# Performance work log

Hardware: AMD Instinct MI355X
Metric: run time of the kernel (lower is better)

Reference implementation:

```python
import jax, jax.numpy as jnp
import numpy as np

PLANE_SIZE = 512
N_LEVELS = 8
FEATURE_DIM = 16
N_PTS = 524288


def setup_inputs() -> dict:
    key = jax.random.key(0)
    k1, k2, k3 = jax.random.split(key, 3)
    x = jax.random.uniform(k1, (N_PTS, 3), dtype=jnp.float32)
    # per-point float mip level bias in [0, n_levels-1]
    level = jax.random.uniform(k2, (N_PTS, 1), dtype=jnp.float32) * (N_LEVELS - 1)
    fm = jax.random.uniform(k3, (3, PLANE_SIZE, PLANE_SIZE, FEATURE_DIM),
                            minval=-0.01, maxval=0.01, dtype=jnp.float32)
    return {"x": x, "level": level, "fm": fm, "n_levels": N_LEVELS}


def _bilinear(flat_pyr, offsets, sizes, uv, lvl_i):
    # flat_pyr: (3, T, C) concatenated mip levels; uv: (3, N, 2); lvl_i: (3, N) int32
    size = sizes[lvl_i]                      # (3, N) texture size at this mip
    fsize = size.astype(uv.dtype)
    px = uv[..., 0] * fsize - 0.5            # u -> width axis (nvdiffrast convention)
    py = uv[..., 1] * fsize - 0.5            # v -> height axis
    x0 = jnp.floor(px)
    y0 = jnp.floor(py)
    fx = (px - x0)[..., None]
    fy = (py - y0)[..., None]
    x0i = x0.astype(jnp.int32)
    y0i = y0.astype(jnp.int32)
    xa = jnp.clip(x0i, 0, size - 1)          # boundary_mode='clamp'
    xb = jnp.clip(x0i + 1, 0, size - 1)
    ya = jnp.clip(y0i, 0, size - 1)
    yb = jnp.clip(y0i + 1, 0, size - 1)
    base = offsets[lvl_i]
    p = jnp.arange(3)[:, None]
    g = lambda yy, xx: flat_pyr[p, base + yy * size + xx]   # (3, N, C) gather
    f00 = g(ya, xa); f01 = g(ya, xb); f10 = g(yb, xa); f11 = g(yb, xb)
    return (f00 * (1 - fx) + f01 * fx) * (1 - fy) + (f10 * (1 - fx) + f11 * fx) * fy


def reference(x, level, fm, n_levels):
    N = x.shape[0]
    C = fm.shape[-1]
    # build mip pyramid via 2x2 box filter (nvdiffrast auto-mips)
    levels = [fm]
    for _ in range(n_levels - 1):
        t = levels[-1]
        s = t.shape[1]
        levels.append(t.reshape(3, s // 2, 2, s // 2, 2, C).mean(axis=(2, 4)))
    sizes_list = [l.shape[1] for l in levels]
    offsets = jnp.asarray(np.cumsum([0] + [s * s for s in sizes_list[:-1]]), jnp.int32)
    sizes = jnp.asarray(sizes_list, jnp.int32)
    flat_pyr = jnp.concatenate([l.reshape(3, -1, C) for l in levels], axis=1)  # (3, T, C)
    # tri-plane decomposition: plane0 sees (y,z), plane1 (x,z), plane2 (x,y)
    uv = jnp.stack([x[:, [1, 2]], x[:, [0, 2]], x[:, [0, 1]]], axis=0)  # (3, N, 2)
    max_mip = n_levels - 1
    lvl = jnp.clip(jnp.broadcast_to(level.reshape(1, N), (3, N)), 0.0, float(max_mip))
    l0 = jnp.floor(lvl)
    f = (lvl - l0)[..., None]                # (3, N, 1) level fraction
    l0i = l0.astype(jnp.int32)
    l1i = jnp.minimum(l0i + 1, max_mip)
    s0 = _bilinear(flat_pyr, offsets, sizes, uv, l0i)
    s1 = _bilinear(flat_pyr, offsets, sizes, uv, l1i)
    enc = s0 * (1 - f) + s1 * f              # (3, N, C) trilinear (mip-lerped)
    # permute(1,2,0,3).view(N, 3C): per point, concat plane0|plane1|plane2 features
    return jnp.transpose(enc, (1, 0, 2)).reshape(N, 3 * C)
```

## Files before the change

kernel.cpp:

```cpp
#include <hip/hip_runtime.h>


#define FM_PLANE_STRIDE (262144 * 16)
#define WS_PLANE_STRIDE (87376 * 16)

__device__ __forceinline__ float4 ld4(const float* p) {
    return *reinterpret_cast<const float4*>(p);
}
__device__ __forceinline__ void st4(float* p, float4 v) {
    *reinterpret_cast<float4*>(p) = v;
}
__device__ __forceinline__ float4 avg4(float4 a, float4 b, float4 c, float4 d) {
    float4 r;
    r.x = (a.x + b.x + c.x + d.x) * 0.25f;
    r.y = (a.y + b.y + c.y + d.y) * 0.25f;
    r.z = (a.z + b.z + c.z + d.z) * 0.25f;
    r.w = (a.w + b.w + c.w + d.w) * 0.25f;
    return r;
}

__global__ __launch_bounds__(256) void mip_build(
    const float* __restrict__ src, float* __restrict__ dst)
{
    const int s = 256;
    int t = blockIdx.x * blockDim.x + threadIdx.x;
    const int p = blockIdx.y;
    const int q = t & 3;
    const int idx = t >> 2;
    const int y = idx >> 8;
    const int x = idx & 255;
    const int ss = 512;
    const float* sp = src + (size_t)p * FM_PLANE_STRIDE
                          + ((size_t)(2 * y) * ss + 2 * x) * 16 + q * 4;
    float4 a = ld4(sp);
    float4 b = ld4(sp + 16);
    float4 c = ld4(sp + (size_t)ss * 16);
    float4 d = ld4(sp + (size_t)ss * 16 + 16);
    float* dp = dst + (size_t)p * WS_PLANE_STRIDE + ((size_t)y * s + x) * 16 + q * 4;
    st4(dp, avg4(a, b, c, d));
}

__global__ __launch_bounds__(256) void mip_tail(float* __restrict__ mips)
{
    const int tile = blockIdx.x;
    const int q    = blockIdx.y;
    const int p    = blockIdx.z;
    const int ty = tile >> 2, tx = tile & 3;
    const int tid = threadIdx.x;

    __shared__ float4 A[32 * 32];
    __shared__ float4 B[16 * 16];

    float* plane = mips + (size_t)p * WS_PLANE_STRIDE;
    const float* L1 = plane;
    float* L2 = plane + (size_t)65536 * 16;
    float* L3 = plane + (size_t)81920 * 16;
    float* L4 = plane + (size_t)86016 * 16;
    float* L5 = plane + (size_t)87040 * 16;
    float* L6 = plane + (size_t)87296 * 16;
    float* L7 = plane + (size_t)87360 * 16;

    #pragma unroll
    for (int k = 0; k < 4; ++k) {
        int li = tid + k * 256;
        int ly = li >> 5, lx = li & 31;
        int gy = ty * 32 + ly, gx = tx * 32 + lx;
        const float* sp = L1 + ((size_t)(2 * gy) * 256 + 2 * gx) * 16 + q * 4;
        float4 r = avg4(ld4(sp), ld4(sp + 16),
                        ld4(sp + 256 * 16), ld4(sp + 256 * 16 + 16));
        A[li] = r;
        st4(L2 + ((size_t)gy * 128 + gx) * 16 + q * 4, r);
    }
    __syncthreads();

    if (tid < 256) {
        int ly = tid >> 4, lx = tid & 15;
        float4 r = avg4(A[(2 * ly) * 32 + 2 * lx],     A[(2 * ly) * 32 + 2 * lx + 1],
                        A[(2 * ly + 1) * 32 + 2 * lx], A[(2 * ly + 1) * 32 + 2 * lx + 1]);
        B[tid] = r;
        st4(L3 + ((size_t)(ty * 16 + ly) * 64 + tx * 16 + lx) * 16 + q * 4, r);
    }
    __syncthreads();

    if (tid < 64) {
        int ly = tid >> 3, lx = tid & 7;
        float4 r = avg4(B[(2 * ly) * 16 + 2 * lx],     B[(2 * ly) * 16 + 2 * lx + 1],
                        B[(2 * ly + 1) * 16 + 2 * lx], B[(2 * ly + 1) * 16 + 2 * lx + 1]);
        A[tid] = r;
        st4(L4 + ((size_t)(ty * 8 + ly) * 32 + tx * 8 + lx) * 16 + q * 4, r);
    }
    __syncthreads();

    if (tid < 16) {
        int ly = tid >> 2, lx = tid & 3;
        float4 r = avg4(A[(2 * ly) * 8 + 2 * lx],     A[(2 * ly) * 8 + 2 * lx + 1],
                        A[(2 * ly + 1) * 8 + 2 * lx], A[(2 * ly + 1) * 8 + 2 * lx + 1]);
        B[tid] = r;
        st4(L5 + ((size_t)(ty * 4 + ly) * 16 + tx * 4 + lx) * 16 + q * 4, r);
    }
    __syncthreads();

    if (tid < 4) {
        int ly = tid >> 1, lx = tid & 1;
        float4 r = avg4(B[(2 * ly) * 4 + 2 * lx],     B[(2 * ly) * 4 + 2 * lx + 1],
                        B[(2 * ly + 1) * 4 + 2 * lx], B[(2 * ly + 1) * 4 + 2 * lx + 1]);
        A[tid] = r;
        st4(L6 + ((size_t)(ty * 2 + ly) * 8 + tx * 2 + lx) * 16 + q * 4, r);
    }
    __syncthreads();

    if (tid == 0) {
        float4 r = avg4(A[0], A[1], A[2], A[3]);
        st4(L7 + ((size_t)ty * 4 + tx) * 16 + q * 4, r);
    }
}

__device__ __forceinline__ float4 bilerp(
    const float* __restrict__ fm, const float* __restrict__ mips,
    int p, int l, float u, float v, int q)
{
    const int sz = 512 >> l;
    const float fsz = (float)sz;
    float px = u * fsz - 0.5f;
    float py = v * fsz - 0.5f;
    float xf = floorf(px);
    float yf = floorf(py);
    float fx = px - xf;
    float fy = py - yf;
    int xi = (int)xf;
    int yi = (int)yf;
    int xa = min(max(xi, 0), sz - 1);
    int xb = min(xi + 1, sz - 1);
    int ya = min(max(yi, 0), sz - 1);
    int yb = min(yi + 1, sz - 1);
    const float* base;
    if (l == 0) {
        base = fm + (size_t)p * FM_PLANE_STRIDE;
    } else {
        unsigned off = (262144u - ((unsigned)(sz * sz) << 2)) / 3u;
        base = mips + (size_t)p * WS_PLANE_STRIDE + (size_t)off * 16;
    }
    const float* r0 = base + (size_t)(ya * sz) * 16 + q * 4;
    const float* r1 = base + (size_t)(yb * sz) * 16 + q * 4;
    float4 f00 = ld4(r0 + xa * 16);
    float4 f01 = ld4(r0 + xb * 16);
    float4 f10 = ld4(r1 + xa * 16);
    float4 f11 = ld4(r1 + xb * 16);
    float gx = 1.f - fx, gy = 1.f - fy;
    float4 r;
    r.x = (f00.x * gx + f01.x * fx) * gy + (f10.x * gx + f11.x * fx) * fy;
    r.y = (f00.y * gx + f01.y * fx) * gy + (f10.y * gx + f11.y * fx) * fy;
    r.z = (f00.z * gx + f01.z * fx) * gy + (f10.z * gx + f11.z * fx) * fy;
    r.w = (f00.w * gx + f01.w * fx) * gy + (f10.w * gx + f11.w * fx) * fy;
    return r;
}

__global__ __launch_bounds__(256) void trimip_sample(
    const float* __restrict__ xyz, const float* __restrict__ level,
    const float* __restrict__ fm, const float* __restrict__ mips,
    float* __restrict__ out, int N)
{
    int t = blockIdx.x * blockDim.x + threadIdx.x;
    if (t >= N * 12) return;
    const int q = t & 3;
    const int r = t >> 2;
    const int n = r / 3;
    const int p = r - n * 3;

    const float c0 = xyz[n * 3 + 0];
    const float c1 = xyz[n * 3 + 1];
    const float c2 = xyz[n * 3 + 2];
    const float u = (p == 0) ? c1 : c0;
    const float v = (p == 2) ? c1 : c2;

    float lv = level[n];
    lv = fminf(fmaxf(lv, 0.f), 7.f);
    float lf = floorf(lv);
    float f = lv - lf;
    int l0 = (int)lf;
    int l1 = min(l0 + 1, 7);

    float4 s0 = bilerp(fm, mips, p, l0, u, v, q);
    float4 s1 = bilerp(fm, mips, p, l1, u, v, q);
    float g = 1.f - f;
    float4 o;
    o.x = s0.x * g + s1.x * f;
    o.y = s0.y * g + s1.y * f;
    o.z = s0.z * g + s1.z * f;
    o.w = s0.w * g + s1.w * f;
    reinterpret_cast<float4*>(out)[t] = o;
}

extern "C" void kernel_launch(void* const* d_in, const int* in_sizes, int n_in,
                              void* d_out, int out_size, void* d_ws, size_t ws_size,
                              hipStream_t stream) {
    const float* xyz   = (const float*)d_in[0];
    const float* level = (const float*)d_in[1];
    const float* fm    = (const float*)d_in[2];
    float* mips = (float*)d_ws;
    float* out  = (float*)d_out;
    const int N = in_sizes[1];

    mip_build<<<dim3(1024, 3), dim3(256), 0, stream>>>(fm, mips);
    mip_tail<<<dim3(16, 4, 3), dim3(256), 0, stream>>>(mips);

    const int total = N * 12;
    const int blocks = (total + 255) / 256;
    trimip_sample<<<blocks, 256, 0, stream>>>(xyz, level, fm, mips, out, N);
}
```

Baseline: 211.2 us.

## Store mip pyramid in fp16 and sample eight channels per thread

Converts the full-resolution feature map and all mip levels into an fp16 copy in the workspace. The sampler then reads half-precision texels with one 16-byte load per corner covering 8 channels, so each thread handles 8 channels instead of 4. Output stores are nontemporal. The aim is to halve gather traffic in the random-access sampling kernel, at the cost of fp16 rounding error and an extra full-resolution conversion write. The fp32 path is kept as a fallback when the workspace is too small.

```diff
diff --git a/kernel.cpp b/kernel.cpp
--- a/kernel.cpp
+++ b/kernel.cpp
@@ -1,46 +1,83 @@
 #include <hip/hip_runtime.h>
-
+#include <hip/hip_fp16.h>
+
+
+typedef float  f4v   __attribute__((ext_vector_type(4)));
+typedef unsigned int u32x2 __attribute__((ext_vector_type(2)));
 
 #define FM_PLANE_STRIDE (262144 * 16)
 #define WS_PLANE_STRIDE (87376 * 16)
-
-__device__ __forceinline__ float4 ld4(const float* p) {
-    return *reinterpret_cast<const float4*>(p);
-}
-__device__ __forceinline__ void st4(float* p, float4 v) {
-    *reinterpret_cast<float4*>(p) = v;
-}
-__device__ __forceinline__ float4 avg4(float4 a, float4 b, float4 c, float4 d) {
-    float4 r;
-    r.x = (a.x + b.x + c.x + d.x) * 0.25f;
-    r.y = (a.y + b.y + c.y + d.y) * 0.25f;
-    r.z = (a.z + b.z + c.z + d.z) * 0.25f;
-    r.w = (a.w + b.w + c.w + d.w) * 0.25f;
+#define PSTRIDE_H (349520 * 16)
+#define WS_H_BYTES (3ull * PSTRIDE_H * 2ull)
+
+__device__ __forceinline__ unsigned lvl_off(int l) {
+    return (1048576u - (1048576u >> (2 * l))) / 3u;
+}
+
+__device__ __forceinline__ f4v ld4(const float* p) {
+    return *reinterpret_cast<const f4v*>(p);
+}
+__device__ __forceinline__ f4v ld4nt(const float* p) {
+    return __builtin_nontemporal_load(reinterpret_cast<const f4v*>(p));
+}
+__device__ __forceinline__ void st4(float* p, f4v v) {
+    *reinterpret_cast<f4v*>(p) = v;
+}
+__device__ __forceinline__ void st4nt(float* p, f4v v) {
+    __builtin_nontemporal_store(v, reinterpret_cast<f4v*>(p));
+}
+__device__ __forceinline__ f4v ldraw_h(const __half* p) {
+    return *reinterpret_cast<const f4v*>(p);
+}
+__device__ __forceinline__ u32x2 pack4(f4v v) {
+    __half2 lo = __floats2half2_rn(v.x, v.y);
+    __half2 hi = __floats2half2_rn(v.z, v.w);
+    u32x2 r;
+    r.x = *reinterpret_cast<unsigned*>(&lo);
+    r.y = *reinterpret_cast<unsigned*>(&hi);
     return r;
 }
-
-__global__ __launch_bounds__(256) void mip_build(
-    const float* __restrict__ src, float* __restrict__ dst)
-{
-    const int s = 256;
-    int t = blockIdx.x * blockDim.x + threadIdx.x;
+__device__ __forceinline__ f4v h4f(const __half* p) {
+    u32x2 u = *reinterpret_cast<const u32x2*>(p);
+    unsigned a0 = u.x, a1 = u.y;
+    __half2 lo = *reinterpret_cast<__half2*>(&a0);
+    __half2 hi = *reinterpret_cast<__half2*>(&a1);
+    float2 flo = __half22float2(lo), fhi = __half22float2(hi);
+    f4v r; r.x = flo.x; r.y = flo.y; r.z = fhi.x; r.w = fhi.y;
+    return r;
+}
+__device__ __forceinline__ float2 up2(float rawcomp) {
+    unsigned u = __float_as_uint(rawcomp);
+    __half2 hh = *reinterpret_cast<__half2*>(&u);
+    return __half22float2(hh);
+}
+
+
+__global__ __launch_bounds__(256) void mip_convert_l1(
+    const float* __restrict__ fm, __half* __restrict__ wsh)
+{
+    int t = blockIdx.x * 256 + threadIdx.x;
     const int p = blockIdx.y;
-    const int q = t & 3;
-    const int idx = t >> 2;
-    const int y = idx >> 8;
-    const int x = idx & 255;
-    const int ss = 512;
-    const float* sp = src + (size_t)p * FM_PLANE_STRIDE
-                          + ((size_t)(2 * y) * ss + 2 * x) * 16 + q * 4;
-    float4 a = ld4(sp);
-    float4 b = ld4(sp + 16);
-    float4 c = ld4(sp + (size_t)ss * 16);
-    float4 d = ld4(sp + (size_t)ss * 16 + 16);
-    float* dp = dst + (size_t)p * WS_PLANE_STRIDE + ((size_t)y * s + x) * 16 + q * 4;
-    st4(dp, avg4(a, b, c, d));
-}
-
-__global__ __launch_bounds__(256) void mip_tail(float* __restrict__ mips)
+    const int q = t & 3, idx = t >> 2;
+    const int y = idx >> 8, x = idx & 255;
+    const float* sp = fm + (size_t)p * FM_PLANE_STRIDE
+                         + ((size_t)(2 * y) * 512 + 2 * x) * 16 + q * 4;
+    f4v a = ld4nt(sp);
+    f4v b = ld4nt(sp + 16);
+    f4v c = ld4nt(sp + 512 * 16);
+    f4v d = ld4nt(sp + 512 * 16 + 16);
+    __half* L0 = wsh + (size_t)p * PSTRIDE_H;
+    size_t o00 = ((size_t)(2 * y) * 512 + 2 * x) * 16 + q * 4;
+    *reinterpret_cast<u32x2*>(L0 + o00)                = pack4(a);
+    *reinterpret_cast<u32x2*>(L0 + o00 + 16)           = pack4(b);
+    *reinterpret_cast<u32x2*>(L0 + o00 + 512 * 16)     = pack4(c);
+    *reinterpret_cast<u32x2*>(L0 + o00 + 512 * 16 + 16) = pack4(d);
+    f4v m = (a + b + c + d) * 0.25f;
+    __half* L1 = wsh + (size_t)p * PSTRIDE_H + (size_t)262144 * 16;
+    *reinterpret_cast<u32x2*>(L1 + ((size_t)y * 256 + x) * 16 + q * 4) = pack4(m);
+}
+
+__global__ __launch_bounds__(256) void mip_tail_h(__half* __restrict__ wsh)
 {
     const int tile = blockIdx.x;
     const int q    = blockIdx.y;
@@ -48,9 +85,166 @@
     const int ty = tile >> 2, tx = tile & 3;
     const int tid = threadIdx.x;
 
-    __shared__ float4 A[32 * 32];
-    __shared__ float4 B[16 * 16];
-
+    __shared__ f4v A[32 * 32];
+    __shared__ f4v B[16 * 16];
+
+    __half* plane = wsh + (size_t)p * PSTRIDE_H;
+    const __half* L1 = plane + (size_t)lvl_off(1) * 16;
+    __half* L2 = plane + (size_t)lvl_off(2) * 16;
+    __half* L3 = plane + (size_t)lvl_off(3) * 16;
+    __half* L4 = plane + (size_t)lvl_off(4) * 16;
+    __half* L5 = plane + (size_t)lvl_off(5) * 16;
+    __half* L6 = plane + (size_t)lvl_off(6) * 16;
+    __half* L7 = plane + (size_t)lvl_off(7) * 16;
+
+    #pragma unroll
+    for (int k = 0; k < 4; ++k) {
+        int li = tid + k * 256;
+        int ly = li >> 5, lx = li & 31;
+        int gy = ty * 32 + ly, gx = tx * 32 + lx;
+        const __half* sp = L1 + ((size_t)(2 * gy) * 256 + 2 * gx) * 16 + q * 4;
+        f4v r = (h4f(sp) + h4f(sp + 16) + h4f(sp + 256 * 16) + h4f(sp + 256 * 16 + 16)) * 0.25f;
+        A[li] = r;
+        *reinterpret_cast<u32x2*>(L2 + ((size_t)gy * 128 + gx) * 16 + q * 4) = pack4(r);
+    }
+    __syncthreads();
+
+    {
+        int ly = tid >> 4, lx = tid & 15;
+        f4v r = (A[(2 * ly) * 32 + 2 * lx]     + A[(2 * ly) * 32 + 2 * lx + 1] +
+                 A[(2 * ly + 1) * 32 + 2 * lx] + A[(2 * ly + 1) * 32 + 2 * lx + 1]) * 0.25f;
+        B[tid] = r;
+        *reinterpret_cast<u32x2*>(L3 + ((size_t)(ty * 16 + ly) * 64 + tx * 16 + lx) * 16 + q * 4) = pack4(r);
+    }
+    __syncthreads();
+
+    if (tid < 64) {
+        int ly = tid >> 3, lx = tid & 7;
+        f4v r = (B[(2 * ly) * 16 + 2 * lx]     + B[(2 * ly) * 16 + 2 * lx + 1] +
+                 B[(2 * ly + 1) * 16 + 2 * lx] + B[(2 * ly + 1) * 16 + 2 * lx + 1]) * 0.25f;
+        A[tid] = r;
+        *reinterpret_cast<u32x2*>(L4 + ((size_t)(ty * 8 + ly) * 32 + tx * 8 + lx) * 16 + q * 4) = pack4(r);
+    }
+    __syncthreads();
+
+    if (tid < 16) {
+        int ly = tid >> 2, lx = tid & 3;
+        f4v r = (A[(2 * ly) * 8 + 2 * lx]     + A[(2 * ly) * 8 + 2 * lx + 1] +
+                 A[(2 * ly + 1) * 8 + 2 * lx] + A[(2 * ly + 1) * 8 + 2 * lx + 1]) * 0.25f;
+        B[tid] = r;
+        *reinterpret_cast<u32x2*>(L5 + ((size_t)(ty * 4 + ly) * 16 + tx * 4 + lx) * 16 + q * 4) = pack4(r);
+    }
+    __syncthreads();
+
+    if (tid < 4) {
+        int ly = tid >> 1, lx = tid & 1;
+        f4v r = (B[(2 * ly) * 4 + 2 * lx]     + B[(2 * ly) * 4 + 2 * lx + 1] +
+                 B[(2 * ly + 1) * 4 + 2 * lx] + B[(2 * ly + 1) * 4 + 2 * lx + 1]) * 0.25f;
+        A[tid] = r;
+        *reinterpret_cast<u32x2*>(L6 + ((size_t)(ty * 2 + ly) * 8 + tx * 2 + lx) * 16 + q * 4) = pack4(r);
+    }
+    __syncthreads();
+
+    if (tid == 0) {
+        f4v r = (A[0] + A[1] + A[2] + A[3]) * 0.25f;
+        *reinterpret_cast<u32x2*>(L7 + ((size_t)ty * 4 + tx) * 16 + q * 4) = pack4(r);
+    }
+}
+
+__device__ __forceinline__ void bilerp8(
+    const __half* __restrict__ wsh, int p, int l, float u, float v, int h, float* o)
+{
+    const int sz = 512 >> l;
+    const float fsz = (float)sz;
+    float px = u * fsz - 0.5f;
+    float py = v * fsz - 0.5f;
+    float xf = floorf(px), yf = floorf(py);
+    float fx = px - xf, fy = py - yf;
+    int xi = (int)xf, yi = (int)yf;
+    int xa = min(max(xi, 0), sz - 1);
+    int xb = min(xi + 1, sz - 1);
+    int ya = min(max(yi, 0), sz - 1);
+    int yb = min(yi + 1, sz - 1);
+    const __half* base = wsh + (size_t)p * PSTRIDE_H + (size_t)lvl_off(l) * 16 + h * 8;
+    const __half* r0 = base + (size_t)(ya * sz) * 16;
+    const __half* r1 = base + (size_t)(yb * sz) * 16;
+    f4v q00 = ldraw_h(r0 + (size_t)xa * 16);
+    f4v q01 = ldraw_h(r0 + (size_t)xb * 16);
+    f4v q10 = ldraw_h(r1 + (size_t)xa * 16);
+    f4v q11 = ldraw_h(r1 + (size_t)xb * 16);
+    float gx = 1.f - fx, gy = 1.f - fy;
+    float w00 = gx * gy, w01 = fx * gy, w10 = gx * fy, w11 = fx * fy;
+    #pragma unroll
+    for (int i = 0; i < 4; ++i) {
+        float2 a = up2(q00[i]), b = up2(q01[i]), c = up2(q10[i]), d = up2(q11[i]);
+        o[2 * i]     = a.x * w00 + b.x * w01 + c.x * w10 + d.x * w11;
+        o[2 * i + 1] = a.y * w00 + b.y * w01 + c.y * w10 + d.y * w11;
+    }
+}
+
+__global__ __launch_bounds__(256) void trimip_sample_h(
+    const float* __restrict__ xyz, const float* __restrict__ level,
+    const __half* __restrict__ wsh, float* __restrict__ out, int N)
+{
+    int t = blockIdx.x * blockDim.x + threadIdx.x;
+    if (t >= N * 6) return;
+    const int h = t & 1;
+    const int r = t >> 1;
+    const int n = r / 3;
+    const int p = r - n * 3;
+
+    const float c0 = xyz[n * 3 + 0];
+    const float c1 = xyz[n * 3 + 1];
+    const float c2 = xyz[n * 3 + 2];
+    const float u = (p == 0) ? c1 : c0;
+    const float v = (p == 2) ? c1 : c2;
+
+    float lv = level[n];
+    lv = fminf(fmaxf(lv, 0.f), 7.f);
+    float lf = floorf(lv);
+    float f = lv - lf;
+    int l0 = (int)lf;
+    int l1 = min(l0 + 1, 7);
+
+    float s0[8], s1[8];
+    bilerp8(wsh, p, l0, u, v, h, s0);
+    bilerp8(wsh, p, l1, u, v, h, s1);
+    float g = 1.f - f;
+    f4v oa, ob;
+    #pragma unroll
+    for (int i = 0; i < 4; ++i) {
+        oa[i] = s0[i] * g + s1[i] * f;
+        ob[i] = s0[4 + i] * g + s1[4 + i] * f;
+    }
+    st4nt(out + (size_t)t * 8, oa);
+    st4nt(out + (size_t)t * 8 + 4, ob);
+}
+
+
+__device__ __forceinline__ f4v avg4(f4v a, f4v b, f4v c, f4v d) {
+    return (a + b + c + d) * 0.25f;
+}
+
+__global__ __launch_bounds__(256) void mip_build_f(
+    const float* __restrict__ src, float* __restrict__ dst)
+{
+    int t = blockIdx.x * blockDim.x + threadIdx.x;
+    const int p = blockIdx.y;
+    const int q = t & 3, idx = t >> 2;
+    const int y = idx >> 8, x = idx & 255;
+    const float* sp = src + (size_t)p * FM_PLANE_STRIDE
+                          + ((size_t)(2 * y) * 512 + 2 * x) * 16 + q * 4;
+    f4v r = avg4(ld4(sp), ld4(sp + 16), ld4(sp + 512 * 16), ld4(sp + 512 * 16 + 16));
+    st4(dst + (size_t)p * WS_PLANE_STRIDE + ((size_t)y * 256 + x) * 16 + q * 4, r);
+}
+
+__global__ __launch_bounds__(256) void mip_tail_f(float* __restrict__ mips)
+{
+    const int tile = blockIdx.x, q = blockIdx.y, p = blockIdx.z;
+    const int ty = tile >> 2, tx = tile & 3;
+    const int tid = threadIdx.x;
+    __shared__ f4v A[32 * 32];
+    __shared__ f4v B[16 * 16];
     float* plane = mips + (size_t)p * WS_PLANE_STRIDE;
     const float* L1 = plane;
     float* L2 = plane + (size_t)65536 * 16;
@@ -66,56 +260,50 @@
         int ly = li >> 5, lx = li & 31;
         int gy = ty * 32 + ly, gx = tx * 32 + lx;
         const float* sp = L1 + ((size_t)(2 * gy) * 256 + 2 * gx) * 16 + q * 4;
-        float4 r = avg4(ld4(sp), ld4(sp + 16),
-                        ld4(sp + 256 * 16), ld4(sp + 256 * 16 + 16));
+        f4v r = avg4(ld4(sp), ld4(sp + 16), ld4(sp + 256 * 16), ld4(sp + 256 * 16 + 16));
         A[li] = r;
         st4(L2 + ((size_t)gy * 128 + gx) * 16 + q * 4, r);
     }
     __syncthreads();
-
-    if (tid < 256) {
+    {
         int ly = tid >> 4, lx = tid & 15;
-        float4 r = avg4(A[(2 * ly) * 32 + 2 * lx],     A[(2 * ly) * 32 + 2 * lx + 1],
-                        A[(2 * ly + 1) * 32 + 2 * lx], A[(2 * ly + 1) * 32 + 2 * lx + 1]);
+        f4v r = avg4(A[(2 * ly) * 32 + 2 * lx],     A[(2 * ly) * 32 + 2 * lx + 1],
+                     A[(2 * ly + 1) * 32 + 2 * lx], A[(2 * ly + 1) * 32 + 2 * lx + 1]);
         B[tid] = r;
         st4(L3 + ((size_t)(ty * 16 + ly) * 64 + tx * 16 + lx) * 16 + q * 4, r);
     }
     __syncthreads();
-
     if (tid < 64) {
         int ly = tid >> 3, lx = tid & 7;
-        float4 r = avg4(B[(2 * ly) * 16 + 2 * lx],     B[(2 * ly) * 16 + 2 * lx + 1],
-                        B[(2 * ly + 1) * 16 + 2 * lx], B[(2 * ly + 1) * 16 + 2 * lx + 1]);
+        f4v r = avg4(B[(2 * ly) * 16 + 2 * lx],     B[(2 * ly) * 16 + 2 * lx + 1],
+                     B[(2 * ly + 1) * 16 + 2 * lx], B[(2 * ly + 1) * 16 + 2 * lx + 1]);
         A[tid] = r;
         st4(L4 + ((size_t)(ty * 8 + ly) * 32 + tx * 8 + lx) * 16 + q * 4, r);
     }
     __syncthreads();
-
     if (tid < 16) {
         int ly = tid >> 2, lx = tid & 3;
-        float4 r = avg4(A[(2 * ly) * 8 + 2 * lx],     A[(2 * ly) * 8 + 2 * lx + 1],
-                        A[(2 * ly + 1) * 8 + 2 * lx], A[(2 * ly + 1) * 8 + 2 * lx + 1]);
+        f4v r = avg4(A[(2 * ly) * 8 + 2 * lx],     A[(2 * ly) * 8 + 2 * lx + 1],
+                     A[(2 * ly + 1) * 8 + 2 * lx], A[(2 * ly + 1) * 8 + 2 * lx + 1]);
         B[tid] = r;
         st4(L5 + ((size_t)(ty * 4 + ly) * 16 + tx * 4 + lx) * 16 + q * 4, r);
     }
     __syncthreads();
-
     if (tid < 4) {
         int ly = tid >> 1, lx = tid & 1;
-        float4 r = avg4(B[(2 * ly) * 4 + 2 * lx],     B[(2 * ly) * 4 + 2 * lx + 1],
-                        B[(2 * ly + 1) * 4 + 2 * lx], B[(2 * ly + 1) * 4 + 2 * lx + 1]);
+        f4v r = avg4(B[(2 * ly) * 4 + 2 * lx],     B[(2 * ly) * 4 + 2 * lx + 1],
+                     B[(2 * ly + 1) * 4 + 2 * lx], B[(2 * ly + 1) * 4 + 2 * lx + 1]);
         A[tid] = r;
         st4(L6 + ((size_t)(ty * 2 + ly) * 8 + tx * 2 + lx) * 16 + q * 4, r);
     }
     __syncthreads();
-
     if (tid == 0) {
-        float4 r = avg4(A[0], A[1], A[2], A[3]);
+        f4v r = avg4(A[0], A[1], A[2], A[3]);
         st4(L7 + ((size_t)ty * 4 + tx) * 16 + q * 4, r);
     }
 }
 
-__device__ __forceinline__ float4 bilerp(
+__device__ __forceinline__ f4v bilerp_f(
     const float* __restrict__ fm, const float* __restrict__ mips,
     int p, int l, float u, float v, int q)
 {
@@ -123,12 +311,9 @@
     const float fsz = (float)sz;
     float px = u * fsz - 0.5f;
     float py = v * fsz - 0.5f;
-    float xf = floorf(px);
-    float yf = floorf(py);
-    float fx = px - xf;
-    float fy = py - yf;
-    int xi = (int)xf;
-    int yi = (int)yf;
+    float xf = floorf(px), yf = floorf(py);
+    float fx = px - xf, fy = py - yf;
+    int xi = (int)xf, yi = (int)yf;
     int xa = min(max(xi, 0), sz - 1);
     int xb = min(xi + 1, sz - 1);
     int ya = min(max(yi, 0), sz - 1);
@@ -142,20 +327,15 @@
     }
     const float* r0 = base + (size_t)(ya * sz) * 16 + q * 4;
     const float* r1 = base + (size_t)(yb * sz) * 16 + q * 4;
-    float4 f00 = ld4(r0 + xa * 16);
-    float4 f01 = ld4(r0 + xb * 16);
-    float4 f10 = ld4(r1 + xa * 16);
-    float4 f11 = ld4(r1 + xb * 16);
+    f4v f00 = ld4(r0 + xa * 16);
+    f4v f01 = ld4(r0 + xb * 16);
+    f4v f10 = ld4(r1 + xa * 16);
+    f4v f11 = ld4(r1 + xb * 16);
     float gx = 1.f - fx, gy = 1.f - fy;
-    float4 r;
-    r.x = (f00.x * gx + f01.x * fx) * gy + (f10.x * gx + f11.x * fx) * fy;
-    r.y = (f00.y * gx + f01.y * fx) * gy + (f10.y * gx + f11.y * fx) * fy;
-    r.z = (f00.z * gx + f01.z * fx) * gy + (f10.z * gx + f11.z * fx) * fy;
-    r.w = (f00.w * gx + f01.w * fx) * gy + (f10.w * gx + f11.w * fx) * fy;
-    return r;
-}
-
-__global__ __launch_bounds__(256) void trimip_sample(
+    return (f00 * gx + f01 * fx) * gy + (f10 * gx + f11 * fx) * fy;
+}
+
+__global__ __launch_bounds__(256) void trimip_sample_f(
     const float* __restrict__ xyz, const float* __restrict__ level,
     const float* __restrict__ fm, const float* __restrict__ mips,
     float* __restrict__ out, int N)
@@ -166,29 +346,21 @@
     const int r = t >> 2;
     const int n = r / 3;
     const int p = r - n * 3;
-
     const float c0 = xyz[n * 3 + 0];
     const float c1 = xyz[n * 3 + 1];
     const float c2 = xyz[n * 3 + 2];
     const float u = (p == 0) ? c1 : c0;
     const float v = (p == 2) ? c1 : c2;
-
     float lv = level[n];
     lv = fminf(fmaxf(lv, 0.f), 7.f);
     float lf = floorf(lv);
     float f = lv - lf;
     int l0 = (int)lf;
     int l1 = min(l0 + 1, 7);
-
-    float4 s0 = bilerp(fm, mips, p, l0, u, v, q);
-    float4 s1 = bilerp(fm, mips, p, l1, u, v, q);
-    float g = 1.f - f;
-    float4 o;
-    o.x = s0.x * g + s1.x * f;
-    o.y = s0.y * g + s1.y * f;
-    o.z = s0.z * g + s1.z * f;
-    o.w = s0.w * g + s1.w * f;
-    reinterpret_cast<float4*>(out)[t] = o;
+    f4v s0 = bilerp_f(fm, mips, p, l0, u, v, q);
+    f4v s1 = bilerp_f(fm, mips, p, l1, u, v, q);
+    f4v o = s0 * (1.f - f) + s1 * f;
+    st4nt(out + (size_t)t * 4, o);
 }
 
 extern "C" void kernel_launch(void* const* d_in, const int* in_sizes, int n_in,
@@ -197,14 +369,20 @@
     const float* xyz   = (const float*)d_in[0];
     const float* level = (const float*)d_in[1];
     const float* fm    = (const float*)d_in[2];
-    float* mips = (float*)d_ws;
-    float* out  = (float*)d_out;
+    float* out = (float*)d_out;
     const int N = in_sizes[1];
 
-    mip_build<<<dim3(1024, 3), dim3(256), 0, stream>>>(fm, mips);
-    mip_tail<<<dim3(16, 4, 3), dim3(256), 0, stream>>>(mips);
-
-    const int total = N * 12;
-    const int blocks = (total + 255) / 256;
-    trimip_sample<<<blocks, 256, 0, stream>>>(xyz, level, fm, mips, out, N);
-}
+    if (ws_size >= WS_H_BYTES) {
+        __half* wsh = (__half*)d_ws;
+        mip_convert_l1<<<dim3(1024, 3), dim3(256), 0, stream>>>(fm, wsh);
+        mip_tail_h<<<dim3(16, 4, 3), dim3(256), 0, stream>>>(wsh);
+        const int total = N * 6;
+        trimip_sample_h<<<(total + 255) / 256, 256, 0, stream>>>(xyz, level, wsh, out, N);
+    } else {
+        float* mips = (float*)d_ws;
+        mip_build_f<<<dim3(1024, 3), dim3(256), 0, stream>>>(fm, mips);
+        mip_tail_f<<<dim3(16, 4, 3), dim3(256), 0, stream>>>(mips);
+        const int total = N * 12;
+        trimip_sample_f<<<(total + 255) / 256, 256, 0, stream>>>(xyz, level, fm, mips, out, N);
+    }
+}
```

New measurement: 203.6 us. -3.6%, faster.
